# Kernel optimization log

Measured on AMD Instinct MI355X. Metric: run time of the kernel, lower is better.

## Reference

```python
import jax, jax.numpy as jnp
import numpy as np

N_NODES = 50000
N_EDGES = 800000
D_IN = 512
D_OUT = 256


def setup_inputs() -> dict:
    key = jax.random.key(0)
    k1, k2, k3 = jax.random.split(key, 3)
    x = jax.random.normal(k1, (N_NODES, D_IN), dtype=jnp.float32)
    edge_index = jax.random.randint(k2, (2, N_EDGES), 0, N_NODES, dtype=jnp.int64)
    # Glorot-style init for the GCN weight, zero bias (PyG defaults)
    W = jax.random.normal(k3, (D_IN, D_OUT), dtype=jnp.float32) * (1.0 / np.sqrt(D_IN))
    b = jnp.zeros((D_OUT,), dtype=jnp.float32)
    return {"x": x, "edge_index": edge_index, "W": W, "b": b}


def reference(x, edge_index, W, b):
    N = x.shape[0]
    # 1) dense linear transform (the compute-heavy GEMM)
    xw = x @ W  # [N, d_out]

    # 2) add self-loops (PyG GCNConv default)
    loop = jnp.arange(N, dtype=edge_index.dtype)
    row = jnp.concatenate([edge_index[0], loop])  # sources
    col = jnp.concatenate([edge_index[1], loop])  # targets

    # 3) symmetric normalization deg^{-1/2} on targets (in-degree incl. self-loops)
    deg = jax.ops.segment_sum(jnp.ones_like(col, dtype=xw.dtype), col, num_segments=N)
    dinv = jnp.where(deg > 0, jax.lax.rsqrt(deg), 0.0)
    norm = dinv[row] * dinv[col]  # [E+N]

    # 4) gather source features, scale, scatter-add to targets
    msgs = xw[row] * norm[:, None]  # [E+N, d_out]
    agg = jax.ops.segment_sum(msgs, col, num_segments=N)  # [N, d_out]

    # 5) bias + ReLU (dropout is identity in eval mode)
    return jax.nn.relu(agg + b)
```

## Files before the change

kernel.cpp:

```cpp
#include <hip/hip_runtime.h>
#include <hip/hip_bf16.h>

#define N_NODES 50000
#define N_EDGES 800000
#define D_IN    512
#define D_OUT   256
#define NBLK_SCAN ((N_NODES + 1023) / 1024)
#define GEMM_NWG (((N_NODES + 127) / 128) * 2)
#define GEMM_Q   (GEMM_NWG / 8)
#define GEMM_R   (GEMM_NWG % 8)

typedef short s8v  __attribute__((ext_vector_type(8)));
typedef float f32x4 __attribute__((ext_vector_type(4)));

__device__ __forceinline__ unsigned short bf16b(float f) {
    __hip_bfloat16 h = __float2bfloat16(f);
    return *reinterpret_cast<unsigned short*>(&h);
}
__device__ __forceinline__ float bflo(unsigned u) { return __uint_as_float(u << 16); }
__device__ __forceinline__ float bfhi(unsigned u) { return __uint_as_float(u & 0xffff0000u); }

#define GLD16(gp, lp)                                                           \
    __builtin_amdgcn_global_load_lds(                                           \
        (const __attribute__((address_space(1))) unsigned int*)(const void*)(gp),\
        (__attribute__((address_space(3))) unsigned int*)(void*)(lp), 16, 0, 0)

__device__ __forceinline__ int wave_incl_scan(int v, int lane) {
    #pragma unroll
    for (int d = 1; d < 64; d <<= 1) {
        int u = __shfl_up(v, d, 64);
        if (lane >= d) v += u;
    }
    return v;
}


__global__ void k_count(const int* __restrict__ col, int* __restrict__ cnt) {
    int i = blockIdx.x * 256 + threadIdx.x;
    if (i < N_EDGES) atomicAdd(&cnt[col[i]], 1);
}

__launch_bounds__(256)
__global__ void k_scan1(const int* __restrict__ cnt, int* __restrict__ bsum) {
    const int t = threadIdx.x, b = blockIdx.x;
    const int idx = b * 1024 + t * 4;
    int4 v = make_int4(0, 0, 0, 0);
    if (idx < N_NODES) v = *(const int4*)&cnt[idx];
    int s = v.x + v.y + v.z + v.w;
    #pragma unroll
    for (int d = 1; d < 64; d <<= 1) s += __shfl_xor(s, d, 64);
    __shared__ int ws[4];
    if ((t & 63) == 0) ws[t >> 6] = s;
    __syncthreads();
    if (t == 0) bsum[b] = ws[0] + ws[1] + ws[2] + ws[3];
}

__global__ void k_scan2(const int* __restrict__ bsum, int* __restrict__ boff) {
    const int t = threadIdx.x;
    int v = (t < NBLK_SCAN) ? bsum[t] : 0;
    int inc = wave_incl_scan(v, t);
    if (t < NBLK_SCAN) boff[t] = inc - v;
}

__launch_bounds__(256)
__global__ void k_scan3(const int* __restrict__ cnt, const int* __restrict__ boff,
                        int* __restrict__ row_ptr, float* __restrict__ dinv,
                        int* __restrict__ cursor) {
    const int t = threadIdx.x, b = blockIdx.x;
    const int lane = t & 63, wv = t >> 6;
    const int idx = b * 1024 + t * 4;
    int4 v = make_int4(0, 0, 0, 0);
    if (idx < N_NODES) v = *(const int4*)&cnt[idx];
    int s = v.x + v.y + v.z + v.w;
    int isc = wave_incl_scan(s, lane);
    __shared__ int wsum[4];
    if (lane == 63) wsum[wv] = isc;
    __syncthreads();
    int off = boff[b];
    #pragma unroll
    for (int i = 0; i < 4; ++i)
        if (i < wv) off += wsum[i];
    int p0 = off + isc - s;
    int p1 = p0 + v.x;
    int p2 = p1 + v.y;
    int p3 = p2 + v.z;
    if (idx < N_NODES) {
        row_ptr[idx + 0] = p0; cursor[idx + 0] = p0; dinv[idx + 0] = rsqrtf(1.f + (float)v.x);
        row_ptr[idx + 1] = p1; cursor[idx + 1] = p1; dinv[idx + 1] = rsqrtf(1.f + (float)v.y);
        row_ptr[idx + 2] = p2; cursor[idx + 2] = p2; dinv[idx + 2] = rsqrtf(1.f + (float)v.z);
        row_ptr[idx + 3] = p3; cursor[idx + 3] = p3; dinv[idx + 3] = rsqrtf(1.f + (float)v.w);
    }
    if (b == 0 && t == 0) row_ptr[N_NODES] = N_EDGES;
}

__global__ void k_fill(const int* __restrict__ row, const int* __restrict__ col,
                       int* __restrict__ cursor, int* __restrict__ csr_src) {
    int i = blockIdx.x * 256 + threadIdx.x;
    if (i < N_EDGES) {
        int pos = atomicAdd(&cursor[col[i]], 1);
        csr_src[pos] = row[i];
    }
}

__global__ void k_wt(const float* __restrict__ W, unsigned short* __restrict__ Wt) {
    int k = blockIdx.x;
    int n = threadIdx.x;
    Wt[(size_t)n * D_IN + k] = bf16b(W[(size_t)k * D_OUT + n]);
}

__launch_bounds__(256)
__global__ void k_gemm(const float* __restrict__ A,
                       const unsigned short* __restrict__ Wt,
                       const float* __restrict__ dinv,
                       unsigned short* __restrict__ yb)
{
    __shared__ __align__(16) float          As[2 * 128 * 32];
    __shared__ __align__(16) unsigned short Bs[2 * 128 * 32];

    int orig = blockIdx.x;
    int xcd = orig % 8, pos = orig / 8;
    int wg = (xcd < GEMM_R) ? xcd * (GEMM_Q + 1) + pos
                            : GEMM_R * (GEMM_Q + 1) + (xcd - GEMM_R) * GEMM_Q + pos;
    const int nt = wg & 1;
    const int mt = wg >> 1;
    const int m0 = mt * 128;
    const int n0 = nt * 128;

    const int t  = threadIdx.x;
    const int w  = t >> 6;
    const int l  = t & 63;
    const int wm = (w >> 1) * 64;
    const int wn = (w & 1) * 64;
    const int lr = l & 15;
    const int lk = l >> 4;

    size_t aoff[4];
    #pragma unroll
    for (int i = 0; i < 4; ++i) {
        int r = m0 + w * 32 + i * 8 + (l >> 3);
        if (r >= N_NODES) r = 0;
        aoff[i] = (size_t)r * D_IN + ((l & 7) ^ (l >> 3)) * 4;
    }
    size_t boff[2];
    #pragma unroll
    for (int i = 0; i < 2; ++i) {
        int r = n0 + w * 32 + i * 16 + (l >> 2);
        boff[i] = (size_t)r * D_IN + ((l & 3) ^ ((l >> 3) & 3)) * 8;
    }

    f32x4 acc[4][4] = {};

    #define STAGE(buf, kk)                                                       \
        do {                                                                     \
            char* ab = (char*)As + (buf) * 16384 + w * 4096;                     \
            char* bb = (char*)Bs + (buf) * 8192  + w * 2048;                     \
            _Pragma("unroll")                                                    \
            for (int i = 0; i < 4; ++i) GLD16(&A[aoff[i] + (kk)], ab + i * 1024);\
            _Pragma("unroll")                                                    \
            for (int i = 0; i < 2; ++i) GLD16(&Wt[boff[i] + (kk)], bb + i * 1024);\
        } while (0)

    #define COMPUTE(buf)                                                         \
        do {                                                                     \
            const char* abase = (const char*)As + (buf) * 16384;                 \
            const char* bbase = (const char*)Bs + (buf) * 8192;                  \
            s8v af[4], bfr[4];                                                   \
            _Pragma("unroll")                                                    \
            for (int f = 0; f < 4; ++f) {                                        \
                int row = wm + f * 16 + lr;                   \
                int s0  = (2 * lk) ^ (lr & 7);                                   \
                const char* pr = abase + row * 128;                              \
                float4 x0 = *(const float4*)(pr + s0 * 16);                      \
                float4 x1 = *(const float4*)(pr + (s0 ^ 1) * 16);                \
                union { s8v v; unsigned short h[8]; } u;                         \
                u.h[0] = bf16b(x0.x); u.h[1] = bf16b(x0.y);                      \
                u.h[2] = bf16b(x0.z); u.h[3] = bf16b(x0.w);                      \
                u.h[4] = bf16b(x1.x); u.h[5] = bf16b(x1.y);                      \
                u.h[6] = bf16b(x1.z); u.h[7] = bf16b(x1.w);                      \
                af[f] = u.v;                                                     \
            }                                                                    \
            _Pragma("unroll")                                                    \
            for (int f = 0; f < 4; ++f) {                                        \
                int row = wn + f * 16 + lr;         \
                int s   = lk ^ ((lr >> 1) & 3);                                  \
                bfr[f] = *(const s8v*)(bbase + row * 64 + s * 16);               \
            }                                                                    \
            _Pragma("unroll")                                                    \
            for (int fm = 0; fm < 4; ++fm)                                       \
                _Pragma("unroll")                                                \
                for (int fn = 0; fn < 4; ++fn)                                   \
                    acc[fm][fn] = __builtin_amdgcn_mfma_f32_16x16x32_bf16(       \
                        af[fm], bfr[fn], acc[fm][fn], 0, 0, 0);                  \
        } while (0)

    STAGE(0, 0);
    __syncthreads();

    #pragma unroll 1
    for (int tk = 0; tk < 15; ++tk) {
        STAGE((tk + 1) & 1, (tk + 1) * 32);
        COMPUTE(tk & 1);
        __syncthreads();
    }
    COMPUTE(1);

    #undef STAGE
    #undef COMPUTE

    #pragma unroll
    for (int fm = 0; fm < 4; ++fm) {
        #pragma unroll
        for (int j = 0; j < 4; ++j) {
            int row = m0 + wm + fm * 16 + lk * 4 + j;
            if (row < N_NODES) {
                float s = dinv[row];
                #pragma unroll
                for (int fn = 0; fn < 4; ++fn) {
                    int col = n0 + wn + fn * 16 + lr;
                    yb[(size_t)row * D_OUT + col] = bf16b(acc[fm][fn][j] * s);
                }
            }
        }
    }
}

__device__ __forceinline__ void add8(float* acc, uint4 q) {
    unsigned x;
    x = q.x; acc[0] += bflo(x); acc[1] += bfhi(x);
    x = q.y; acc[2] += bflo(x); acc[3] += bfhi(x);
    x = q.z; acc[4] += bflo(x); acc[5] += bfhi(x);
    x = q.w; acc[6] += bflo(x); acc[7] += bfhi(x);
}

__launch_bounds__(256)
__global__ void k_gather(const int* __restrict__ row_ptr, const int* __restrict__ csr_src,
                         const unsigned short* __restrict__ yb, const float* __restrict__ dinv,
                         const float* __restrict__ bias, float* __restrict__ out)
{
    const int c  = blockIdx.x * 4 + (threadIdx.x >> 6);
    const int l  = threadIdx.x & 63;
    const int eg = l >> 5;
    const int cs = l & 31;
    const size_t colb = (size_t)cs * 8;

    float acc[8] = {0.f,0.f,0.f,0.f,0.f,0.f,0.f,0.f};

    const int s = row_ptr[c];
    const int e = row_ptr[c + 1];

    int i = s + eg;
    while (i + 14 < e) {
        int r[8];
        #pragma unroll
        for (int u = 0; u < 8; ++u) r[u] = csr_src[i + 2 * u];
        uint4 v[8];
        #pragma unroll
        for (int u = 0; u < 8; ++u) v[u] = *(const uint4*)&yb[(size_t)r[u] * D_OUT + colb];
        #pragma unroll
        for (int u = 0; u < 8; ++u) add8(acc, v[u]);
        i += 16;
    }
    while (i < e) {
        int r[4];
        #pragma unroll
        for (int u = 0; u < 4; ++u) {
            int p = i + 2 * u;
            r[u] = csr_src[p < e ? p : e - 1];
        }
        uint4 v[4];
        #pragma unroll
        for (int u = 0; u < 4; ++u) v[u] = *(const uint4*)&yb[(size_t)r[u] * D_OUT + colb];
        #pragma unroll
        for (int u = 0; u < 4; ++u)
            if (i + 2 * u < e) add8(acc, v[u]);
        i += 8;
    }

    #pragma unroll
    for (int u = 0; u < 8; ++u) acc[u] += __shfl_xor(acc[u], 32, 64);

    uint4 sv = *(const uint4*)&yb[(size_t)c * D_OUT + colb];
    add8(acc, sv);

    if (eg == 0) {
        const float sc = dinv[c];
        float4 b0 = *(const float4*)&bias[colb];
        float4 b1 = *(const float4*)&bias[colb + 4];
        float4 o0, o1;
        o0.x = fmaxf(fmaf(acc[0], sc, b0.x), 0.f);
        o0.y = fmaxf(fmaf(acc[1], sc, b0.y), 0.f);
        o0.z = fmaxf(fmaf(acc[2], sc, b0.z), 0.f);
        o0.w = fmaxf(fmaf(acc[3], sc, b0.w), 0.f);
        o1.x = fmaxf(fmaf(acc[4], sc, b1.x), 0.f);
        o1.y = fmaxf(fmaf(acc[5], sc, b1.y), 0.f);
        o1.z = fmaxf(fmaf(acc[6], sc, b1.z), 0.f);
        o1.w = fmaxf(fmaf(acc[7], sc, b1.w), 0.f);
        float* dst = &out[(size_t)c * D_OUT + colb];
        *(float4*)dst       = o0;
        *(float4*)(dst + 4) = o1;
    }
}

extern "C" void kernel_launch(void* const* d_in, const int* in_sizes, int n_in,
                              void* d_out, int out_size, void* d_ws, size_t ws_size,
                              hipStream_t stream) {
    const float* x   = (const float*)d_in[0];
    const int*   ei  = (const int*)d_in[1];
    const float* W   = (const float*)d_in[2];
    const float* b   = (const float*)d_in[3];
    float*       out = (float*)d_out;

    const int* row = ei;
    const int* col = ei + N_EDGES;

    char* p = (char*)d_ws;
    unsigned short* yb = (unsigned short*)p;  p += (size_t)N_NODES * D_OUT * 2;
    unsigned short* Wt = (unsigned short*)p;  p += (size_t)D_OUT * D_IN * 2;
    int*   csr_src = (int*)p;                 p += (size_t)N_EDGES * 4;
    int*   cnt     = (int*)p;                 p += (size_t)N_NODES * 4;
    int*   row_ptr = (int*)p;                 p += (size_t)(N_NODES + 4) * 4;
    int*   cursor  = (int*)p;                 p += (size_t)N_NODES * 4;
    float* dinv    = (float*)p;               p += (size_t)N_NODES * 4;
    int*   bsum    = (int*)p;                 p += (size_t)NBLK_SCAN * 4;
    int*   boff    = (int*)p;                 p += (size_t)NBLK_SCAN * 4;

    hipMemsetAsync(cnt, 0, (size_t)N_NODES * sizeof(int), stream);
    k_count<<<(N_EDGES + 255) / 256, 256, 0, stream>>>(col, cnt);
    k_scan1<<<NBLK_SCAN, 256, 0, stream>>>(cnt, bsum);
    k_scan2<<<1, 64, 0, stream>>>(bsum, boff);
    k_scan3<<<NBLK_SCAN, 256, 0, stream>>>(cnt, boff, row_ptr, dinv, cursor);
    k_fill <<<(N_EDGES + 255) / 256, 256, 0, stream>>>(row, col, cursor, csr_src);
    k_wt   <<<D_IN, D_OUT, 0, stream>>>(W, Wt);

    k_gemm<<<GEMM_NWG, 256, 0, stream>>>(x, Wt, dinv, yb);

    k_gather<<<N_NODES / 4, 256, 0, stream>>>(row_ptr, csr_src, yb, dinv, b, out);
}
```

Before: 218.7 us.

## Single-buffer GEMM LDS, fold scan2 into scan3, vectorize count/fill edges

```diff
diff --git a/kernel.cpp b/kernel.cpp
--- a/kernel.cpp
+++ b/kernel.cpp
@@ -36,8 +36,12 @@
 
 
 __global__ void k_count(const int* __restrict__ col, int* __restrict__ cnt) {
-    int i = blockIdx.x * 256 + threadIdx.x;
-    if (i < N_EDGES) atomicAdd(&cnt[col[i]], 1);
+    int i = (blockIdx.x * 256 + threadIdx.x) * 2;
+    if (i < N_EDGES) {
+        int2 c = *(const int2*)&col[i];
+        atomicAdd(&cnt[c.x], 1);
+        atomicAdd(&cnt[c.y], 1);
+    }
 }
 
 __launch_bounds__(256)
@@ -55,15 +59,8 @@
     if (t == 0) bsum[b] = ws[0] + ws[1] + ws[2] + ws[3];
 }
 
-__global__ void k_scan2(const int* __restrict__ bsum, int* __restrict__ boff) {
-    const int t = threadIdx.x;
-    int v = (t < NBLK_SCAN) ? bsum[t] : 0;
-    int inc = wave_incl_scan(v, t);
-    if (t < NBLK_SCAN) boff[t] = inc - v;
-}
-
 __launch_bounds__(256)
-__global__ void k_scan3(const int* __restrict__ cnt, const int* __restrict__ boff,
+__global__ void k_scan3(const int* __restrict__ cnt, const int* __restrict__ bsum,
                         int* __restrict__ row_ptr, float* __restrict__ dinv,
                         int* __restrict__ cursor) {
     const int t = threadIdx.x, b = blockIdx.x;
@@ -74,9 +71,16 @@
     int s = v.x + v.y + v.z + v.w;
     int isc = wave_incl_scan(s, lane);
     __shared__ int wsum[4];
+    __shared__ int s_boff;
     if (lane == 63) wsum[wv] = isc;
+    if (t < 64) {
+        int u = (t < b) ? bsum[t] : 0;
+        #pragma unroll
+        for (int d = 1; d < 64; d <<= 1) u += __shfl_xor(u, d, 64);
+        if (t == 0) s_boff = u;
+    }
     __syncthreads();
-    int off = boff[b];
+    int off = s_boff;
     #pragma unroll
     for (int i = 0; i < 4; ++i)
         if (i < wv) off += wsum[i];
@@ -95,10 +99,14 @@
 
 __global__ void k_fill(const int* __restrict__ row, const int* __restrict__ col,
                        int* __restrict__ cursor, int* __restrict__ csr_src) {
-    int i = blockIdx.x * 256 + threadIdx.x;
+    int i = (blockIdx.x * 256 + threadIdx.x) * 2;
     if (i < N_EDGES) {
-        int pos = atomicAdd(&cursor[col[i]], 1);
-        csr_src[pos] = row[i];
+        int2 c = *(const int2*)&col[i];
+        int2 r = *(const int2*)&row[i];
+        int p0 = atomicAdd(&cursor[c.x], 1);
+        csr_src[p0] = r.x;
+        int p1 = atomicAdd(&cursor[c.y], 1);
+        csr_src[p1] = r.y;
     }
 }
 
@@ -114,8 +122,8 @@
                        const float* __restrict__ dinv,
                        unsigned short* __restrict__ yb)
 {
-    __shared__ __align__(16) float          As[2 * 128 * 32];
-    __shared__ __align__(16) unsigned short Bs[2 * 128 * 32];
+    __shared__ __align__(16) float          As[128 * 32];
+    __shared__ __align__(16) unsigned short Bs[128 * 32];
 
     int orig = blockIdx.x;
     int xcd = orig % 8, pos = orig / 8;
@@ -150,62 +158,49 @@
 
     f32x4 acc[4][4] = {};
 
-    #define STAGE(buf, kk)                                                       \
-        do {                                                                     \
-            char* ab = (char*)As + (buf) * 16384 + w * 4096;                     \
-            char* bb = (char*)Bs + (buf) * 8192  + w * 2048;                     \
-            _Pragma("unroll")                                                    \
-            for (int i = 0; i < 4; ++i) GLD16(&A[aoff[i] + (kk)], ab + i * 1024);\
-            _Pragma("unroll")                                                    \
-            for (int i = 0; i < 2; ++i) GLD16(&Wt[boff[i] + (kk)], bb + i * 1024);\
-        } while (0)
-
-    #define COMPUTE(buf)                                                         \
-        do {                                                                     \
-            const char* abase = (const char*)As + (buf) * 16384;                 \
-            const char* bbase = (const char*)Bs + (buf) * 8192;                  \
-            s8v af[4], bfr[4];                                                   \
-            _Pragma("unroll")                                                    \
-            for (int f = 0; f < 4; ++f) {                                        \
-                int row = wm + f * 16 + lr;                   \
-                int s0  = (2 * lk) ^ (lr & 7);                                   \
-                const char* pr = abase + row * 128;                              \
-                float4 x0 = *(const float4*)(pr + s0 * 16);                      \
-                float4 x1 = *(const float4*)(pr + (s0 ^ 1) * 16);                \
-                union { s8v v; unsigned short h[8]; } u;                         \
-                u.h[0] = bf16b(x0.x); u.h[1] = bf16b(x0.y);                      \
-                u.h[2] = bf16b(x0.z); u.h[3] = bf16b(x0.w);                      \
-                u.h[4] = bf16b(x1.x); u.h[5] = bf16b(x1.y);                      \
-                u.h[6] = bf16b(x1.z); u.h[7] = bf16b(x1.w);                      \
-                af[f] = u.v;                                                     \
-            }                                                                    \
-            _Pragma("unroll")                                                    \
-            for (int f = 0; f < 4; ++f) {                                        \
-                int row = wn + f * 16 + lr;         \
-                int s   = lk ^ ((lr >> 1) & 3);                                  \
-                bfr[f] = *(const s8v*)(bbase + row * 64 + s * 16);               \
-            }                                                                    \
-            _Pragma("unroll")                                                    \
-            for (int fm = 0; fm < 4; ++fm)                                       \
-                _Pragma("unroll")                                                \
-                for (int fn = 0; fn < 4; ++fn)                                   \
-                    acc[fm][fn] = __builtin_amdgcn_mfma_f32_16x16x32_bf16(       \
-                        af[fm], bfr[fn], acc[fm][fn], 0, 0, 0);                  \
-        } while (0)
-
-    STAGE(0, 0);
-    __syncthreads();
-
     #pragma unroll 1
-    for (int tk = 0; tk < 15; ++tk) {
-        STAGE((tk + 1) & 1, (tk + 1) * 32);
-        COMPUTE(tk & 1);
+    for (int tk = 0; tk < 16; ++tk) {
+        const int kk = tk * 32;
+        {
+            char* ab = (char*)As + w * 4096;
+            char* bb = (char*)Bs + w * 2048;
+            #pragma unroll
+            for (int i = 0; i < 4; ++i) GLD16(&A[aoff[i] + kk], ab + i * 1024);
+            #pragma unroll
+            for (int i = 0; i < 2; ++i) GLD16(&Wt[boff[i] + kk], bb + i * 1024);
+        }
         __syncthreads();
-    }
-    COMPUTE(1);
-
-    #undef STAGE
-    #undef COMPUTE
+        {
+            s8v af[4], bfr[4];
+            #pragma unroll
+            for (int f = 0; f < 4; ++f) {
+                int row = wm + f * 16 + lr;
+                int s0  = (2 * lk) ^ (lr & 7);
+                const char* pr = (const char*)As + row * 128;
+                float4 x0 = *(const float4*)(pr + s0 * 16);
+                float4 x1 = *(const float4*)(pr + (s0 ^ 1) * 16);
+                union { s8v v; unsigned short h[8]; } u;
+                u.h[0] = bf16b(x0.x); u.h[1] = bf16b(x0.y);
+                u.h[2] = bf16b(x0.z); u.h[3] = bf16b(x0.w);
+                u.h[4] = bf16b(x1.x); u.h[5] = bf16b(x1.y);
+                u.h[6] = bf16b(x1.z); u.h[7] = bf16b(x1.w);
+                af[f] = u.v;
+            }
+            #pragma unroll
+            for (int f = 0; f < 4; ++f) {
+                int row = wn + f * 16 + lr;
+                int s   = lk ^ ((lr >> 1) & 3);
+                bfr[f] = *(const s8v*)((const char*)Bs + row * 64 + s * 16);
+            }
+            #pragma unroll
+            for (int fm = 0; fm < 4; ++fm)
+                #pragma unroll
+                for (int fn = 0; fn < 4; ++fn)
+                    acc[fm][fn] = __builtin_amdgcn_mfma_f32_16x16x32_bf16(
+                        af[fm], bfr[fn], acc[fm][fn], 0, 0, 0);
+        }
+        __syncthreads();
+    }
 
     #pragma unroll
     for (int fm = 0; fm < 4; ++fm) {
@@ -322,14 +317,12 @@
     int*   cursor  = (int*)p;                 p += (size_t)N_NODES * 4;
     float* dinv    = (float*)p;               p += (size_t)N_NODES * 4;
     int*   bsum    = (int*)p;                 p += (size_t)NBLK_SCAN * 4;
-    int*   boff    = (int*)p;                 p += (size_t)NBLK_SCAN * 4;
 
     hipMemsetAsync(cnt, 0, (size_t)N_NODES * sizeof(int), stream);
-    k_count<<<(N_EDGES + 255) / 256, 256, 0, stream>>>(col, cnt);
+    k_count<<<(N_EDGES / 2 + 255) / 256, 256, 0, stream>>>(col, cnt);
     k_scan1<<<NBLK_SCAN, 256, 0, stream>>>(cnt, bsum);
-    k_scan2<<<1, 64, 0, stream>>>(bsum, boff);
-    k_scan3<<<NBLK_SCAN, 256, 0, stream>>>(cnt, boff, row_ptr, dinv, cursor);
-    k_fill <<<(N_EDGES + 255) / 256, 256, 0, stream>>>(row, col, cursor, csr_src);
+    k_scan3<<<NBLK_SCAN, 256, 0, stream>>>(cnt, bsum, row_ptr, dinv, cursor);
+    k_fill <<<(N_EDGES / 2 + 255) / 256, 256, 0, stream>>>(row, col, cursor, csr_src);
     k_wt   <<<D_IN, D_OUT, 0, stream>>>(W, Wt);
 
     k_gemm<<<GEMM_NWG, 256, 0, stream>>>(x, Wt, dinv, yb);
```

After: 209.2 us. -4.4%, faster.
